# Kernel optimization log

Measured on AMD Instinct MI355X. Metric: run time of the kernel, lower is better.

## Reference

```python
import jax, jax.numpy as jnp
import numpy as np

B, A, G = 256, 64, 978          # batch, n_atoms, num_gene
D_DRUG, D_CELL, D_DOSE = 128, 50, 128
CELL_IN, DOSE_IN = 978, 12
GLOBAL = D_DRUG + D_CELL + D_DOSE   # 306
EXP_IN = GLOBAL + 128               # 434
E, TOP_K = 4, 2


def setup_inputs() -> dict:
    key = jax.random.key(0)
    ks = jax.random.split(key, 24)
    w = lambda k, s: jax.random.normal(k, s, jnp.float32) * 0.05
    return {
        "drug_atom_embed": jax.random.normal(ks[0], (B, A, D_DRUG), jnp.float32),
        "input_cell_gex": jax.random.normal(ks[1], (B, CELL_IN), jnp.float32),
        "input_pert_idose": jax.random.normal(ks[2], (B, DOSE_IN), jnp.float32),
        # LinearEncoder: 978 -> 200 -> 100 -> 50 (ReLU after each)
        "cell_W1": w(ks[3], (CELL_IN, 200)), "cell_b1": jnp.zeros((200,), jnp.float32),
        "cell_W2": w(ks[4], (200, 100)),     "cell_b2": jnp.zeros((100,), jnp.float32),
        "cell_W3": w(ks[5], (100, D_CELL)),  "cell_b3": jnp.zeros((D_CELL,), jnp.float32),
        # DoseEncoder: 12 -> 64 -> 128 (ReLU after each; dropout off at eval)
        "dose_W1": w(ks[6], (DOSE_IN, 64)),  "dose_b1": jnp.zeros((64,), jnp.float32),
        "dose_W2": w(ks[7], (64, D_DOSE)),   "dose_b2": jnp.zeros((D_DOSE,), jnp.float32),
        # gene index embedding [num_gene, 128]
        "gene_emb": w(ks[8], (G, 128)),
        # GatingNetwork: 306 -> 128 -> 4
        "gate_W1": w(ks[9], (GLOBAL, 128)),  "gate_b1": jnp.zeros((128,), jnp.float32),
        "gate_W2": w(ks[10], (128, E)),      "gate_b2": jnp.zeros((E,), jnp.float32),
        # 4 ExpertNetworks stacked: 434 -> 128 -> 1
        "exp_W1": w(ks[11], (E, EXP_IN, 128)), "exp_b1": jnp.zeros((E, 128), jnp.float32),
        "exp_W2": w(ks[12], (E, 128, 1)),      "exp_b2": jnp.zeros((E, 1), jnp.float32),
    }


def reference(drug_atom_embed, input_cell_gex, input_pert_idose,
              cell_W1, cell_b1, cell_W2, cell_b2, cell_W3, cell_b3,
              dose_W1, dose_b1, dose_W2, dose_b2, gene_emb,
              gate_W1, gate_b1, gate_W2, gate_b2,
              exp_W1, exp_b1, exp_W2, exp_b2):
    relu = jax.nn.relu
    # drug: sum atom embeddings -> [B, 128]
    drug = drug_atom_embed.sum(axis=1)
    # cell encoder -> [B, 50]
    cell = relu(input_cell_gex @ cell_W1 + cell_b1)
    cell = relu(cell @ cell_W2 + cell_b2)
    cell = relu(cell @ cell_W3 + cell_b3)
    # dose encoder -> [B, 128]
    dose = relu(input_pert_idose @ dose_W1 + dose_b1)
    dose = relu(dose @ dose_W2 + dose_b2)
    # global features [B, 306]
    g = jnp.concatenate([drug, cell, dose], axis=1)
    # gating: top-k sparse gates [B, E]
    logits = relu(g @ gate_W1 + gate_b1) @ gate_W2 + gate_b2
    top_v, top_i = jax.lax.top_k(logits, TOP_K)
    top_g = jax.nn.softmax(top_v, axis=1)
    gates = jnp.zeros_like(logits).at[jnp.arange(logits.shape[0])[:, None], top_i].set(top_g)
    # gene-aware expert input [B, G, 434]
    expert_input = jnp.concatenate([
        jnp.broadcast_to(g[:, None, :], (g.shape[0], G, GLOBAL)),
        jnp.broadcast_to(gene_emb[None, :, :], (g.shape[0], G, 128)),
    ], axis=2)
    # all experts: [B, E, G, 128] -> [B, E, G]
    h = relu(jnp.einsum('bgi,eih->begh', expert_input, exp_W1) + exp_b1[None, :, None, :])
    o = jnp.einsum('begh,eho->beg', h, exp_W2) + exp_b2[None, :, :1]  # exp_b2[e,0] broadcast
    predictions = jnp.einsum('beg,be->bg', o, gates)
    return predictions, cell
```

## Files before the change

### kernel.cpp

```cpp
#include <hip/hip_runtime.h>

#define NB 256
#define NA 64
#define NG 978
#define CELL_IN 978
#define DOSE_IN 12
#define GLOBAL_F 306
#define EXP_IN 434
#define NE 4

#define WS_GATES 0
#define WS_U     (WS_GATES + NB*NE)
#define WS_V     (WS_U + NB*NE*128)

__device__ __forceinline__ float wave_reduce(float p) {
    #pragma unroll
    for (int off = 32; off > 0; off >>= 1) p += __shfl_down(p, off, 64);
    return p;
}

__global__ __launch_bounds__(256) void a_kernel(
    const float* __restrict__ gene, const float* __restrict__ eW1,
    float* __restrict__ ws)
{
    __shared__ float s_gene[128];
    __shared__ float s_p[4 * 2 * 128];
    const int g = blockIdx.x, tid = threadIdx.x;

    if (tid < 128) s_gene[tid] = gene[g * 128 + tid];
    __syncthreads();

    const int e = tid >> 6, ks = (tid >> 5) & 1, h4 = tid & 31;
    const float* wp = eW1 + ((size_t)e * EXP_IN + GLOBAL_F) * 128 + 4 * h4;
    float4 acc = {0.f, 0.f, 0.f, 0.f};
    const int k0 = ks * 64;
    #pragma unroll 8
    for (int k = k0; k < k0 + 64; ++k) {
        float4 w = *(const float4*)(wp + (size_t)k * 128);
        float x = s_gene[k];
        acc.x += x * w.x; acc.y += x * w.y; acc.z += x * w.z; acc.w += x * w.w;
    }
    *(float4*)(s_p + (e * 2 + ks) * 128 + 4 * h4) = acc;
    __syncthreads();

    if (tid < 128) {
        int oe = tid >> 5, oh4 = tid & 31;
        float4 p0 = *(const float4*)(s_p + (oe * 2 + 0) * 128 + 4 * oh4);
        float4 p1 = *(const float4*)(s_p + (oe * 2 + 1) * 128 + 4 * oh4);
        float4 o = {p0.x + p1.x, p0.y + p1.y, p0.z + p1.z, p0.w + p1.w};
        *(float4*)(ws + WS_V + (size_t)g * 512 + oe * 128 + 4 * oh4) = o;
    }
}

__global__ __launch_bounds__(1024) void b_kernel(
    const float* __restrict__ drug, const float* __restrict__ gex,
    const float* __restrict__ idose,
    const float* __restrict__ cW1, const float* __restrict__ cb1,
    const float* __restrict__ cW2, const float* __restrict__ cb2,
    const float* __restrict__ cW3, const float* __restrict__ cb3,
    const float* __restrict__ dW1, const float* __restrict__ db1,
    const float* __restrict__ dW2, const float* __restrict__ db2,
    const float* __restrict__ gW1, const float* __restrict__ gb1,
    const float* __restrict__ gW2, const float* __restrict__ gb2,
    const float* __restrict__ eW1, const float* __restrict__ eb1,
    float* __restrict__ ws, float* __restrict__ cell_out)
{
    __shared__ float s_gex[CELL_IN];
    __shared__ float s_g[GLOBAL_F];
    __shared__ float s_h1[200];
    __shared__ float s_h2[100];
    __shared__ float s_gh[128];
    __shared__ float s_d1[64];
    __shared__ float s_part[16 * 200];
    __shared__ float s_pu[8 * 512];

    const int b = blockIdx.x, tid = threadIdx.x;

    if (tid < CELL_IN) s_gex[tid] = gex[b * CELL_IN + tid];
    {
        int row = tid >> 7, d = tid & 127;
        const float* p = drug + ((size_t)b * NA) * 128 + d;
        float acc = 0.f;
        #pragma unroll
        for (int i = 0; i < 8; ++i) acc += p[(size_t)(i * 8 + row) * 128];
        s_pu[row * 128 + d] = acc;
    }
    __syncthreads();
    if (tid < 128) {
        float a = 0.f;
        #pragma unroll
        for (int r = 0; r < 8; ++r) a += s_pu[r * 128 + tid];
        s_g[tid] = a;
    } else if (tid < 192) {
        int j = tid - 128;
        float acc = db1[j];
        #pragma unroll
        for (int i = 0; i < DOSE_IN; ++i)
            acc += idose[b * DOSE_IN + i] * dW1[i * 64 + j];
        s_d1[j] = fmaxf(acc, 0.f);
    }
    __syncthreads();
    if (tid < 128) {
        float acc = db2[tid];
        #pragma unroll 8
        for (int i = 0; i < 64; ++i) acc += s_d1[i] * dW2[i * 128 + tid];
        s_g[178 + tid] = fmaxf(acc, 0.f);
    }
    __syncthreads();

    {
        int q = tid & 63, ks = tid >> 6;
        if (q < 50) {
            int i0 = ks * 62, i1 = min(i0 + 62, CELL_IN);
            float4 acc = {0.f, 0.f, 0.f, 0.f};
            #pragma unroll 4
            for (int i = i0; i < i1; ++i) {
                float4 w = *(const float4*)(cW1 + (size_t)i * 200 + 4 * q);
                float x = s_gex[i];
                acc.x += x * w.x; acc.y += x * w.y; acc.z += x * w.z; acc.w += x * w.w;
            }
            *(float4*)(s_part + ks * 200 + 4 * q) = acc;
        }
    }
    __syncthreads();
    if (tid < 200) {
        float a = cb1[tid];
        #pragma unroll
        for (int ks = 0; ks < 16; ++ks) a += s_part[ks * 200 + tid];
        s_h1[tid] = fmaxf(a, 0.f);
    }
    __syncthreads();

    {
        int q = tid & 31, ks = tid >> 5;
        if (q < 25 && ks < 16) {
            int i0 = ks * 13, i1 = min(i0 + 13, 200);
            float4 acc = {0.f, 0.f, 0.f, 0.f};
            #pragma unroll
            for (int i = i0; i < i1; ++i) {
                float4 w = *(const float4*)(cW2 + (size_t)i * 100 + 4 * q);
                float x = s_h1[i];
                acc.x += x * w.x; acc.y += x * w.y; acc.z += x * w.z; acc.w += x * w.w;
            }
            *(float4*)(s_part + ks * 100 + 4 * q) = acc;
        }
    }
    __syncthreads();
    if (tid < 100) {
        float a = cb2[tid];
        #pragma unroll
        for (int ks = 0; ks < 16; ++ks) a += s_part[ks * 100 + tid];
        s_h2[tid] = fmaxf(a, 0.f);
    }
    __syncthreads();

    {
        int j = tid & 63, ks = tid >> 6;
        if (j < 50 && ks < 8) {
            int i0 = ks * 13, i1 = min(i0 + 13, 100);
            float acc = 0.f;
            #pragma unroll
            for (int i = i0; i < i1; ++i) acc += s_h2[i] * cW3[i * 50 + j];
            s_part[ks * 64 + j] = acc;
        }
    }
    __syncthreads();
    if (tid < 50) {
        float a = cb3[tid];
        #pragma unroll
        for (int ks = 0; ks < 8; ++ks) a += s_part[ks * 64 + tid];
        float r = fmaxf(a, 0.f);
        s_g[128 + tid] = r;
        cell_out[b * 50 + tid] = r;
    }
    __syncthreads();

    {
        int q = tid & 31, ks = tid >> 5;
        if (ks < 16) {
            int i0 = ks * 20, i1 = min(i0 + 20, GLOBAL_F);
            float4 acc = {0.f, 0.f, 0.f, 0.f};
            #pragma unroll
            for (int i = i0; i < i1; ++i) {
                float4 w = *(const float4*)(gW1 + (size_t)i * 128 + 4 * q);
                float x = s_g[i];
                acc.x += x * w.x; acc.y += x * w.y; acc.z += x * w.z; acc.w += x * w.w;
            }
            *(float4*)(s_part + ks * 128 + 4 * q) = acc;
        }
    }
    __syncthreads();
    if (tid < 128) {
        float a = gb1[tid];
        #pragma unroll
        for (int ks = 0; ks < 16; ++ks) a += s_part[ks * 128 + tid];
        s_gh[tid] = fmaxf(a, 0.f);
    }
    __syncthreads();

    if (tid < 64) {
        float h0 = s_gh[tid], h1 = s_gh[tid + 64];
        float logit[NE];
        #pragma unroll
        for (int j = 0; j < NE; ++j) {
            float p = h0 * gW2[tid * NE + j] + h1 * gW2[(tid + 64) * NE + j];
            p = wave_reduce(p);
            logit[j] = p + gb2[j];
        }
        if (tid == 0) {
            int i1 = 0; float v1 = logit[0];
            #pragma unroll
            for (int i = 1; i < NE; ++i) if (logit[i] > v1) { v1 = logit[i]; i1 = i; }
            int i2 = -1; float v2 = -__builtin_inff();
            #pragma unroll
            for (int i = 0; i < NE; ++i) {
                if (i == i1) continue;
                if (logit[i] > v2) { v2 = logit[i]; i2 = i; }
            }
            float e2 = __expf(v2 - v1);
            float inv = 1.f / (1.f + e2);
            float out[NE] = {0.f, 0.f, 0.f, 0.f};
            out[i1] = inv; out[i2] = e2 * inv;
            #pragma unroll
            for (int i = 0; i < NE; ++i) ws[WS_GATES + b * NE + i] = out[i];
        }
    }
    __syncthreads();

    {
        int e = tid >> 8, ks = (tid >> 5) & 7, h4 = tid & 31;
        int i0 = ks * 39, i1 = min(i0 + 39, GLOBAL_F);
        const float* wp = eW1 + (size_t)e * EXP_IN * 128 + 4 * h4;
        float4 acc = {0.f, 0.f, 0.f, 0.f};
        #pragma unroll 4
        for (int i = i0; i < i1; ++i) {
            float4 w = *(const float4*)(wp + (size_t)i * 128);
            float x = s_g[i];
            acc.x += x * w.x; acc.y += x * w.y; acc.z += x * w.z; acc.w += x * w.w;
        }
        *(float4*)(s_pu + (e * 8 + ks) * 128 + 4 * h4) = acc;
    }
    __syncthreads();
    if (tid < 128) {
        int e = tid >> 5, h4 = tid & 31;
        float4 a = *(const float4*)(eb1 + e * 128 + 4 * h4);
        #pragma unroll
        for (int ks = 0; ks < 8; ++ks) {
            float4 p = *(const float4*)(s_pu + (e * 8 + ks) * 128 + 4 * h4);
            a.x += p.x; a.y += p.y; a.z += p.z; a.w += p.w;
        }
        *(float4*)(ws + WS_U + (size_t)b * 512 + e * 128 + 4 * h4) = a;
    }
}

__global__ __launch_bounds__(256) void c_kernel(
    const float* __restrict__ eW2, const float* __restrict__ eb2,
    const float* __restrict__ ws, float* __restrict__ pred)
{
    __shared__ float s_u[2 * 128];
    __shared__ float s_w2[2 * 128];
    const int b = blockIdx.x >> 2, qt = blockIdx.x & 3, tid = threadIdx.x;

    float g0 = ws[WS_GATES + b * NE + 0], g1 = ws[WS_GATES + b * NE + 1];
    float g2 = ws[WS_GATES + b * NE + 2], g3 = ws[WS_GATES + b * NE + 3];
    float gv[NE] = {g0, g1, g2, g3};
    int e1 = -1, e2 = -1;
    #pragma unroll
    for (int i = 0; i < NE; ++i)
        if (gv[i] > 0.f) { if (e1 < 0) e1 = i; else e2 = i; }
    if (e1 < 0) e1 = 0;
    if (e2 < 0) e2 = (e1 + 1) & 3;
    const float gA = gv[e1], gB = gv[e2];
    const float bA = eb2[e1], bB = eb2[e2];

    if (tid < 256) {
        int es = tid >> 7, h = tid & 127;
        int e = es ? e2 : e1;
        s_u[es * 128 + h] = ws[WS_U + (size_t)b * 512 + e * 128 + h];
        s_w2[es * 128 + h] = eW2[e * 128 + h];
    }
    __syncthreads();

    const int g = qt * 245 + tid;
    if (tid < 245 && g < NG) {
        const float4* vA = (const float4*)(ws + WS_V + (size_t)g * 512 + e1 * 128);
        const float4* vB = (const float4*)(ws + WS_V + (size_t)g * 512 + e2 * 128);
        float dA = 0.f, dB = 0.f;
        #pragma unroll 8
        for (int k = 0; k < 32; ++k) {
            float4 va = vA[k], vb = vB[k];
            dA += fmaxf(s_u[4*k+0] + va.x, 0.f) * s_w2[4*k+0]
                + fmaxf(s_u[4*k+1] + va.y, 0.f) * s_w2[4*k+1]
                + fmaxf(s_u[4*k+2] + va.z, 0.f) * s_w2[4*k+2]
                + fmaxf(s_u[4*k+3] + va.w, 0.f) * s_w2[4*k+3];
            dB += fmaxf(s_u[128+4*k+0] + vb.x, 0.f) * s_w2[128+4*k+0]
                + fmaxf(s_u[128+4*k+1] + vb.y, 0.f) * s_w2[128+4*k+1]
                + fmaxf(s_u[128+4*k+2] + vb.z, 0.f) * s_w2[128+4*k+2]
                + fmaxf(s_u[128+4*k+3] + vb.w, 0.f) * s_w2[128+4*k+3];
        }
        pred[b * NG + g] = gA * (dA + bA) + gB * (dB + bB);
    }
}

extern "C" void kernel_launch(void* const* d_in, const int* in_sizes, int n_in,
                              void* d_out, int out_size, void* d_ws, size_t ws_size,
                              hipStream_t stream) {
    const float* drug  = (const float*)d_in[0];
    const float* gex   = (const float*)d_in[1];
    const float* idose = (const float*)d_in[2];
    const float* cW1 = (const float*)d_in[3];  const float* cb1 = (const float*)d_in[4];
    const float* cW2 = (const float*)d_in[5];  const float* cb2 = (const float*)d_in[6];
    const float* cW3 = (const float*)d_in[7];  const float* cb3 = (const float*)d_in[8];
    const float* dW1 = (const float*)d_in[9];  const float* db1 = (const float*)d_in[10];
    const float* dW2 = (const float*)d_in[11]; const float* db2 = (const float*)d_in[12];
    const float* gene = (const float*)d_in[13];
    const float* gW1 = (const float*)d_in[14]; const float* gb1 = (const float*)d_in[15];
    const float* gW2 = (const float*)d_in[16]; const float* gb2 = (const float*)d_in[17];
    const float* eW1 = (const float*)d_in[18]; const float* eb1 = (const float*)d_in[19];
    const float* eW2 = (const float*)d_in[20]; const float* eb2 = (const float*)d_in[21];

    float* ws   = (float*)d_ws;
    float* out  = (float*)d_out;
    float* pred = out;
    float* cell = out + NB * NG;

    a_kernel<<<NG, 256, 0, stream>>>(gene, eW1, ws);
    b_kernel<<<NB, 1024, 0, stream>>>(drug, gex, idose,
        cW1, cb1, cW2, cb2, cW3, cb3, dW1, db1, dW2, db2,
        gW1, gb1, gW2, gb2, eW1, eb1, ws, cell);
    c_kernel<<<NB * 4, 256, 0, stream>>>(eW2, eb2, ws, pred);
}
```

Baseline: 176.1 us.

## Merge gene and batch precompute kernels, compute only selected experts, tile final stage

Folds the per-gene projection kernel into the batch kernel as extra blocks, so one launch covers both and they run concurrently. The batch part now computes the U projection only for the two top-k experts, storing expert indices and gate weights instead of dense gates. The final kernel is retiled into batch-by-gene tiles that stage V, U and W2 in shared memory, so each V row is reused across 16 batch rows instead of being reloaded per batch. The cost is larger shared memory per block, a heavier block shape for the merged kernel, and per-thread expert indexing with possible LDS bank conflicts.

Measured after the change: 167.3 us. -5.0%, faster.

```diff
diff --git a/kernel.cpp b/kernel.cpp
--- a/kernel.cpp
+++ b/kernel.cpp
@@ -9,9 +9,11 @@
 #define EXP_IN 434
 #define NE 4
 
-#define WS_GATES 0
-#define WS_U     (WS_GATES + NB*NE)
-#define WS_V     (WS_U + NB*NE*128)
+#define WS_SEL 0
+#define WS_U   (WS_SEL + NB*4)
+#define WS_V   (WS_U + NB*256)
+
+#define AB_GRID (NB + 245)
 
 __device__ __forceinline__ float wave_reduce(float p) {
     #pragma unroll
@@ -19,40 +21,7 @@
     return p;
 }
 
-__global__ __launch_bounds__(256) void a_kernel(
-    const float* __restrict__ gene, const float* __restrict__ eW1,
-    float* __restrict__ ws)
-{
-    __shared__ float s_gene[128];
-    __shared__ float s_p[4 * 2 * 128];
-    const int g = blockIdx.x, tid = threadIdx.x;
-
-    if (tid < 128) s_gene[tid] = gene[g * 128 + tid];
-    __syncthreads();
-
-    const int e = tid >> 6, ks = (tid >> 5) & 1, h4 = tid & 31;
-    const float* wp = eW1 + ((size_t)e * EXP_IN + GLOBAL_F) * 128 + 4 * h4;
-    float4 acc = {0.f, 0.f, 0.f, 0.f};
-    const int k0 = ks * 64;
-    #pragma unroll 8
-    for (int k = k0; k < k0 + 64; ++k) {
-        float4 w = *(const float4*)(wp + (size_t)k * 128);
-        float x = s_gene[k];
-        acc.x += x * w.x; acc.y += x * w.y; acc.z += x * w.z; acc.w += x * w.w;
-    }
-    *(float4*)(s_p + (e * 2 + ks) * 128 + 4 * h4) = acc;
-    __syncthreads();
-
-    if (tid < 128) {
-        int oe = tid >> 5, oh4 = tid & 31;
-        float4 p0 = *(const float4*)(s_p + (oe * 2 + 0) * 128 + 4 * oh4);
-        float4 p1 = *(const float4*)(s_p + (oe * 2 + 1) * 128 + 4 * oh4);
-        float4 o = {p0.x + p1.x, p0.y + p1.y, p0.z + p1.z, p0.w + p1.w};
-        *(float4*)(ws + WS_V + (size_t)g * 512 + oe * 128 + 4 * oh4) = o;
-    }
-}
-
-__global__ __launch_bounds__(1024) void b_kernel(
+__global__ __launch_bounds__(1024) void ab_kernel(
     const float* __restrict__ drug, const float* __restrict__ gex,
     const float* __restrict__ idose,
     const float* __restrict__ cW1, const float* __restrict__ cb1,
@@ -63,6 +32,7 @@
     const float* __restrict__ gW1, const float* __restrict__ gb1,
     const float* __restrict__ gW2, const float* __restrict__ gb2,
     const float* __restrict__ eW1, const float* __restrict__ eb1,
+    const float* __restrict__ gene,
     float* __restrict__ ws, float* __restrict__ cell_out)
 {
     __shared__ float s_gex[CELL_IN];
@@ -71,10 +41,42 @@
     __shared__ float s_h2[100];
     __shared__ float s_gh[128];
     __shared__ float s_d1[64];
+    __shared__ int   s_isel[2];
     __shared__ float s_part[16 * 200];
-    __shared__ float s_pu[8 * 512];
-
-    const int b = blockIdx.x, tid = threadIdx.x;
+    __shared__ float s_pu[32 * 128];
+    __shared__ float s_ag[4][128];
+    __shared__ float s_ap[4][8][128];
+
+    const int blk = blockIdx.x, tid = threadIdx.x;
+
+    if (blk >= NB) {
+        const int gq = tid >> 8, lt = tid & 255;
+        const int g = (blk - NB) * 4 + gq;
+        if (lt < 128) s_ag[gq][lt] = (g < NG) ? gene[g * 128 + lt] : 0.f;
+        __syncthreads();
+        const int e = lt >> 6, ks = (lt >> 5) & 1, h4 = lt & 31;
+        const float* wp = eW1 + ((size_t)e * EXP_IN + GLOBAL_F) * 128 + 4 * h4;
+        float4 acc = {0.f, 0.f, 0.f, 0.f};
+        const int k0 = ks * 64;
+        #pragma unroll 8
+        for (int k = k0; k < k0 + 64; ++k) {
+            float4 w = *(const float4*)(wp + (size_t)k * 128);
+            float x = s_ag[gq][k];
+            acc.x += x * w.x; acc.y += x * w.y; acc.z += x * w.z; acc.w += x * w.w;
+        }
+        *(float4*)(&s_ap[gq][e * 2 + ks][4 * h4]) = acc;
+        __syncthreads();
+        if (lt < 128 && g < NG) {
+            int oe = lt >> 5, oh4 = lt & 31;
+            float4 p0 = *(const float4*)(&s_ap[gq][oe * 2 + 0][4 * oh4]);
+            float4 p1 = *(const float4*)(&s_ap[gq][oe * 2 + 1][4 * oh4]);
+            float4 o = {p0.x + p1.x, p0.y + p1.y, p0.z + p1.z, p0.w + p1.w};
+            *(float4*)(ws + WS_V + (size_t)g * 512 + oe * 128 + 4 * oh4) = o;
+        }
+        return;
+    }
+
+    const int b = blk;
 
     if (tid < CELL_IN) s_gex[tid] = gex[b * CELL_IN + tid];
     {
@@ -119,7 +121,7 @@
                 float x = s_gex[i];
                 acc.x += x * w.x; acc.y += x * w.y; acc.z += x * w.z; acc.w += x * w.w;
             }
-            *(float4*)(s_part + ks * 200 + 4 * q) = acc;
+            *(float4*)(&s_part[ks * 200 + 4 * q]) = acc;
         }
     }
     __syncthreads();
@@ -142,7 +144,7 @@
                 float x = s_h1[i];
                 acc.x += x * w.x; acc.y += x * w.y; acc.z += x * w.z; acc.w += x * w.w;
             }
-            *(float4*)(s_part + ks * 100 + 4 * q) = acc;
+            *(float4*)(&s_part[ks * 100 + 4 * q]) = acc;
         }
     }
     __syncthreads();
@@ -186,7 +188,7 @@
                 float x = s_g[i];
                 acc.x += x * w.x; acc.y += x * w.y; acc.z += x * w.z; acc.w += x * w.w;
             }
-            *(float4*)(s_part + ks * 128 + 4 * q) = acc;
+            *(float4*)(&s_part[ks * 128 + 4 * q]) = acc;
         }
     }
     __syncthreads();
@@ -217,88 +219,102 @@
                 if (i == i1) continue;
                 if (logit[i] > v2) { v2 = logit[i]; i2 = i; }
             }
-            float e2 = __expf(v2 - v1);
-            float inv = 1.f / (1.f + e2);
-            float out[NE] = {0.f, 0.f, 0.f, 0.f};
-            out[i1] = inv; out[i2] = e2 * inv;
-            #pragma unroll
-            for (int i = 0; i < NE; ++i) ws[WS_GATES + b * NE + i] = out[i];
-        }
-    }
-    __syncthreads();
-
-    {
-        int e = tid >> 8, ks = (tid >> 5) & 7, h4 = tid & 31;
-        int i0 = ks * 39, i1 = min(i0 + 39, GLOBAL_F);
+            float ex = __expf(v2 - v1);
+            float inv = 1.f / (1.f + ex);
+            s_isel[0] = i1; s_isel[1] = i2;
+            ws[WS_SEL + b * 4 + 0] = (float)i1;
+            ws[WS_SEL + b * 4 + 1] = (float)i2;
+            ws[WS_SEL + b * 4 + 2] = inv;
+            ws[WS_SEL + b * 4 + 3] = ex * inv;
+        }
+    }
+    __syncthreads();
+
+    {
+        int es = tid >> 9, ks = (tid >> 5) & 15, h4 = tid & 31;
+        int e = s_isel[es];
+        int i0 = ks * 20, i1 = min(i0 + 20, GLOBAL_F);
         const float* wp = eW1 + (size_t)e * EXP_IN * 128 + 4 * h4;
         float4 acc = {0.f, 0.f, 0.f, 0.f};
-        #pragma unroll 4
+        #pragma unroll
         for (int i = i0; i < i1; ++i) {
             float4 w = *(const float4*)(wp + (size_t)i * 128);
             float x = s_g[i];
             acc.x += x * w.x; acc.y += x * w.y; acc.z += x * w.z; acc.w += x * w.w;
         }
-        *(float4*)(s_pu + (e * 8 + ks) * 128 + 4 * h4) = acc;
-    }
-    __syncthreads();
-    if (tid < 128) {
-        int e = tid >> 5, h4 = tid & 31;
-        float4 a = *(const float4*)(eb1 + e * 128 + 4 * h4);
-        #pragma unroll
-        for (int ks = 0; ks < 8; ++ks) {
-            float4 p = *(const float4*)(s_pu + (e * 8 + ks) * 128 + 4 * h4);
-            a.x += p.x; a.y += p.y; a.z += p.z; a.w += p.w;
-        }
-        *(float4*)(ws + WS_U + (size_t)b * 512 + e * 128 + 4 * h4) = a;
+        *(float4*)(&s_pu[(es * 16 + ks) * 128 + 4 * h4]) = acc;
+    }
+    __syncthreads();
+    if (tid < 256) {
+        int es = tid >> 7, h = tid & 127;
+        int e = s_isel[es];
+        float a = eb1[e * 128 + h];
+        #pragma unroll
+        for (int ks = 0; ks < 16; ++ks) a += s_pu[(es * 16 + ks) * 128 + h];
+        ws[WS_U + (size_t)b * 256 + es * 128 + h] = a;
     }
 }
 
+#define GT 28
+#define BT 16
 __global__ __launch_bounds__(256) void c_kernel(
     const float* __restrict__ eW2, const float* __restrict__ eb2,
     const float* __restrict__ ws, float* __restrict__ pred)
 {
-    __shared__ float s_u[2 * 128];
-    __shared__ float s_w2[2 * 128];
-    const int b = blockIdx.x >> 2, qt = blockIdx.x & 3, tid = threadIdx.x;
-
-    float g0 = ws[WS_GATES + b * NE + 0], g1 = ws[WS_GATES + b * NE + 1];
-    float g2 = ws[WS_GATES + b * NE + 2], g3 = ws[WS_GATES + b * NE + 3];
-    float gv[NE] = {g0, g1, g2, g3};
-    int e1 = -1, e2 = -1;
+    __shared__ float s_v[GT * 520];
+    __shared__ float s_u[BT * 260];
+    __shared__ float s_w2[512];
+    __shared__ float s_sel[BT * 4];
+    const int bt = blockIdx.x & 15, gt = blockIdx.x >> 4, tid = threadIdx.x;
+    const int b0 = bt * BT, g0 = gt * GT;
+
+    if (tid < BT * 4) s_sel[tid] = ws[WS_SEL + b0 * 4 + tid];
+    for (int i = tid; i < 512; i += 256) s_w2[i] = eW2[i];
+    for (int i4 = tid; i4 < BT * 64; i4 += 256) {
+        int bl = i4 >> 6, h4 = i4 & 63;
+        float4 u = *(const float4*)(ws + WS_U + (size_t)(b0 + bl) * 256 + 4 * h4);
+        *(float4*)(&s_u[bl * 260 + 4 * h4]) = u;
+    }
+    for (int i4 = tid; i4 < GT * 128; i4 += 256) {
+        int gl = i4 >> 7, h4 = i4 & 127;
+        int g = g0 + gl;
+        float4 v = {0.f, 0.f, 0.f, 0.f};
+        if (g < NG) v = *(const float4*)(ws + WS_V + (size_t)g * 512 + 4 * h4);
+        *(float4*)(&s_v[gl * 520 + 4 * h4]) = v;
+    }
+    __syncthreads();
+
+    const int bl = tid & 15;
+    const int ea = (int)s_sel[bl * 4 + 0], eb = (int)s_sel[bl * 4 + 1];
+    const float gA = s_sel[bl * 4 + 2], gB = s_sel[bl * 4 + 3];
+    const float bA = eb2[ea], bB = eb2[eb];
     #pragma unroll
-    for (int i = 0; i < NE; ++i)
-        if (gv[i] > 0.f) { if (e1 < 0) e1 = i; else e2 = i; }
-    if (e1 < 0) e1 = 0;
-    if (e2 < 0) e2 = (e1 + 1) & 3;
-    const float gA = gv[e1], gB = gv[e2];
-    const float bA = eb2[e1], bB = eb2[e2];
-
-    if (tid < 256) {
-        int es = tid >> 7, h = tid & 127;
-        int e = es ? e2 : e1;
-        s_u[es * 128 + h] = ws[WS_U + (size_t)b * 512 + e * 128 + h];
-        s_w2[es * 128 + h] = eW2[e * 128 + h];
-    }
-    __syncthreads();
-
-    const int g = qt * 245 + tid;
-    if (tid < 245 && g < NG) {
-        const float4* vA = (const float4*)(ws + WS_V + (size_t)g * 512 + e1 * 128);
-        const float4* vB = (const float4*)(ws + WS_V + (size_t)g * 512 + e2 * 128);
-        float dA = 0.f, dB = 0.f;
-        #pragma unroll 8
-        for (int k = 0; k < 32; ++k) {
-            float4 va = vA[k], vb = vB[k];
-            dA += fmaxf(s_u[4*k+0] + va.x, 0.f) * s_w2[4*k+0]
-                + fmaxf(s_u[4*k+1] + va.y, 0.f) * s_w2[4*k+1]
-                + fmaxf(s_u[4*k+2] + va.z, 0.f) * s_w2[4*k+2]
-                + fmaxf(s_u[4*k+3] + va.w, 0.f) * s_w2[4*k+3];
-            dB += fmaxf(s_u[128+4*k+0] + vb.x, 0.f) * s_w2[128+4*k+0]
-                + fmaxf(s_u[128+4*k+1] + vb.y, 0.f) * s_w2[128+4*k+1]
-                + fmaxf(s_u[128+4*k+2] + vb.z, 0.f) * s_w2[128+4*k+2]
-                + fmaxf(s_u[128+4*k+3] + vb.w, 0.f) * s_w2[128+4*k+3];
-        }
-        pred[b * NG + g] = gA * (dA + bA) + gB * (dB + bB);
+    for (int it = 0; it < 2; ++it) {
+        int gl = (tid >> 4) + 16 * it;
+        int g = g0 + gl;
+        if (gl < GT && g < NG) {
+            const float* vA = s_v + gl * 520 + ea * 128;
+            const float* vB = s_v + gl * 520 + eb * 128;
+            const float* uA = s_u + bl * 260;
+            const float* uB = uA + 128;
+            const float* wA = s_w2 + ea * 128;
+            const float* wB = s_w2 + eb * 128;
+            float dA = 0.f, dB = 0.f;
+            #pragma unroll 8
+            for (int k = 0; k < 32; ++k) {
+                float4 va = *(const float4*)(vA + 4 * k);
+                float4 ua = *(const float4*)(uA + 4 * k);
+                float4 wa = *(const float4*)(wA + 4 * k);
+                dA += fmaxf(ua.x + va.x, 0.f) * wa.x + fmaxf(ua.y + va.y, 0.f) * wa.y
+                    + fmaxf(ua.z + va.z, 0.f) * wa.z + fmaxf(ua.w + va.w, 0.f) * wa.w;
+                float4 vb = *(const float4*)(vB + 4 * k);
+                float4 ub = *(const float4*)(uB + 4 * k);
+                float4 wb = *(const float4*)(wB + 4 * k);
+                dB += fmaxf(ub.x + vb.x, 0.f) * wb.x + fmaxf(ub.y + vb.y, 0.f) * wb.y
+                    + fmaxf(ub.z + vb.z, 0.f) * wb.z + fmaxf(ub.w + vb.w, 0.f) * wb.w;
+            }
+            pred[(size_t)(b0 + bl) * NG + g] = gA * (dA + bA) + gB * (dB + bB);
+        }
     }
 }
 
@@ -324,9 +340,8 @@
     float* pred = out;
     float* cell = out + NB * NG;
 
-    a_kernel<<<NG, 256, 0, stream>>>(gene, eW1, ws);
-    b_kernel<<<NB, 1024, 0, stream>>>(drug, gex, idose,
+    ab_kernel<<<AB_GRID, 1024, 0, stream>>>(drug, gex, idose,
         cW1, cb1, cW2, cb2, cW3, cb3, dW1, db1, dW2, db2,
-        gW1, gb1, gW2, gb2, eW1, eb1, ws, cell);
-    c_kernel<<<NB * 4, 256, 0, stream>>>(eW2, eb2, ws, pred);
+        gW1, gb1, gW2, gb2, eW1, eb1, gene, ws, cell);
+    c_kernel<<<16 * 35, 256, 0, stream>>>(eW2, eb2, ws, pred);
 }
```
